# Kernel tuning notes

Measured on AMD Instinct MI355X. Metric: run time of the kernel, lower is better.

## Reference

```python
import jax, jax.numpy as jnp
import numpy as np

B, H, W = 16, 16, 16
L = 32          # in_capsules
O = 32          # out_capsules
P = 16          # p_size
PD = 4          # p_dim = sqrt(p_size)
ETA = 1.0


def setup_inputs() -> dict:
    key = jax.random.key(0)
    k1, k2, k3 = jax.random.split(key, 3)
    # [B, H, W, L*(P+1)]: first L*P channels are poses, last L are activations in [0,1]
    input_tensor = jax.random.uniform(k1, (B, H, W, L * (P + 1)), dtype=jnp.float32)
    # transform weights: [L, O, 4, 4] (kernel_size=1, shared over spatial positions)
    weights = jax.random.normal(k2, (L, O, PD, PD), dtype=jnp.float32) / np.sqrt(PD)
    activation_bias = jax.random.uniform(k3, (O,), dtype=jnp.float32)
    return {"input_tensor": input_tensor, "weights": weights,
            "activation_bias": activation_bias}


def reference(input_tensor, weights, activation_bias):
    Bs, Hh, Ww, _ = input_tensor.shape
    M = Hh * Ww
    # split poses / activations
    poses = input_tensor[..., : L * P].reshape(Bs, M, L, PD, PD)   # [B, M, L, 4, 4]
    acts = input_tensor[..., L * P:].reshape(Bs, M * L)            # [B, N]
    # votes[b, (m,l), o] = pose[b,m,l] @ W[l,o]  (shared transform, repeated over M)
    votes = jnp.einsum('bmlij,lojk->bmloik', poses, weights)
    votes = votes.reshape(Bs, M * L, O, P)                         # [B, N, O, 16]
    # weight votes by input activations and group per output capsule
    Y = (acts[:, :, None, None] * votes).transpose(0, 2, 1, 3)     # [B, O, N, 16]
    # top-1 right singular vector via gram matrix eigendecomposition (detached)
    gram = jnp.einsum('bonp,bonq->bopq', Y, Y)                     # [B, O, 16, 16]
    _, V = jnp.linalg.eigh(jax.lax.stop_gradient(gram))            # ascending eigvals
    pose_out = V[..., -1]                                          # [B, O, 16]
    # agreement: ||Y u||^2 / ||Y||_F^2
    yu = jnp.einsum('bonp,bop->bon', Y, pose_out)                  # [B, O, N]
    ratio = (yu ** 2).sum(-1) / (Y ** 2).sum((-1, -2))             # [B, O]
    act_out = jax.nn.sigmoid(ETA * (ratio - activation_bias))      # [B, O]
    return act_out, pose_out
```

## Files before the change

kernel.cpp:

```cpp
#include <hip/hip_runtime.h>

#define B_ 16
#define L_ 32
#define O_ 32
#define M_ 256
#define CH_ 544


__device__ __forceinline__ float rl(float v, int lane) {
  return __int_as_float(__builtin_amdgcn_readlane(__float_as_int(v), lane));
}

__device__ __forceinline__ float sum16_rl(float v) {
  float s = rl(v, 0);
#pragma unroll
  for (int j = 1; j < 16; j++) s += rl(v, j);
  return s;
}

__device__ __forceinline__ float frcp(float x) { return __builtin_amdgcn_rcpf(x); }
__device__ __forceinline__ float frsq(float x) { return __builtin_amdgcn_rsqf(x); }


__device__ __forceinline__ float slapy2f(float x, float y) {
  float xa = fabsf(x), ya = fabsf(y);
  float w = fmaxf(xa, ya), z = fminf(xa, ya);
  float q = z * frcp(w);
  float res = w * sqrtf(1.f + q * q);
  return (z == 0.f) ? w : res;
}

__device__ __forceinline__ void slartgf(float f, float g, float* c, float* s, float* r) {
  float t = f * f + g * g;
  float inv = frsq(t);
  float d = t * inv;
  float cg = fabsf(f) * inv;
  float rg = copysignf(d, f);
  float sg = g * copysignf(inv, f);
  bool g0 = (g == 0.f), f0 = (f == 0.f);
  *c = g0 ? 1.f : (f0 ? 0.f : cg);
  *s = g0 ? 0.f : (f0 ? copysignf(1.f, g) : sg);
  *r = g0 ? f : (f0 ? fabsf(g) : rg);
}

__device__ __forceinline__ void slaev2f(float a, float b, float c,
                                        float* rt1, float* rt2, float* cs1, float* sn1) {
  float sm = a + c, df = a - c;
  float adf = fabsf(df);
  float tb = b + b;
  float ab = fabsf(tb);
  float acmx, acmn;
  if (fabsf(a) > fabsf(c)) { acmx = a; acmn = c; } else { acmx = c; acmn = a; }
  float rt;
  if (adf > ab) { float q = ab / adf; rt = adf * sqrtf(1.f + q * q); }
  else if (adf < ab) { float q = adf / ab; rt = ab * sqrtf(1.f + q * q); }
  else rt = ab * sqrtf(2.f);
  int sgn1;
  if (sm < 0.f) { *rt1 = 0.5f * (sm - rt); sgn1 = -1; *rt2 = (acmx / *rt1) * acmn - (b / *rt1) * b; }
  else if (sm > 0.f) { *rt1 = 0.5f * (sm + rt); sgn1 = 1; *rt2 = (acmx / *rt1) * acmn - (b / *rt1) * b; }
  else { *rt1 = 0.5f * rt; *rt2 = -0.5f * rt; sgn1 = 1; }
  float cs; int sgn2;
  if (df >= 0.f) { cs = df + rt; sgn2 = 1; } else { cs = df - rt; sgn2 = -1; }
  float acs = fabsf(cs), c1, s1;
  if (acs > ab) { float ct = -tb / cs; s1 = 1.f / sqrtf(1.f + ct * ct); c1 = ct * s1; }
  else if (ab == 0.f) { c1 = 1.f; s1 = 0.f; }
  else { float tn = -cs / tb; c1 = 1.f / sqrtf(1.f + tn * tn); s1 = tn * c1; }
  if (sgn1 == sgn2) { float tn = c1; c1 = -s1; s1 = tn; }
  *cs1 = c1; *sn1 = s1;
}

__global__ __launch_bounds__(256) void moments_kernel(const float* __restrict__ in,
                                                      float* __restrict__ Tmom) {
  int bl = blockIdx.x;
  int b = bl >> 5, l = bl & 31;
  int t = threadIdx.x;
  int w = t >> 6, lane = t & 63;
  __shared__ __align__(16) float ut[4][16][68];
  __shared__ float red[4][16][16];
  const float* base = in + (size_t)b * (M_ * CH_);
  const float* row = base + (size_t)(w * 64 + lane) * CH_ + l * 16;
  float4 p0 = *(const float4*)(row + 0);
  float4 p1 = *(const float4*)(row + 4);
  float4 p2 = *(const float4*)(row + 8);
  float4 p3 = *(const float4*)(row + 12);
  float a = row[512 - l * 16 + l];
  float (*u)[68] = ut[w];
  u[0][lane] = a * p0.x;  u[1][lane] = a * p0.y;  u[2][lane] = a * p0.z;  u[3][lane] = a * p0.w;
  u[4][lane] = a * p1.x;  u[5][lane] = a * p1.y;  u[6][lane] = a * p1.z;  u[7][lane] = a * p1.w;
  u[8][lane] = a * p2.x;  u[9][lane] = a * p2.y;  u[10][lane] = a * p2.z; u[11][lane] = a * p2.w;
  u[12][lane] = a * p3.x; u[13][lane] = a * p3.y; u[14][lane] = a * p3.z; u[15][lane] = a * p3.w;
  asm volatile("" ::: "memory");
  int c = lane & 15, r0 = lane >> 4;
  float acc0 = 0.f, acc1 = 0.f, acc2 = 0.f, acc3 = 0.f;
#pragma unroll
  for (int m4 = 0; m4 < 64; m4 += 4) {
    float4 cv = *(const float4*)&u[c][m4];
    float4 a0 = *(const float4*)&u[r0][m4];
    float4 a1 = *(const float4*)&u[r0 + 4][m4];
    float4 a2 = *(const float4*)&u[r0 + 8][m4];
    float4 a3 = *(const float4*)&u[r0 + 12][m4];
    acc0 += a0.x * cv.x + a0.y * cv.y + a0.z * cv.z + a0.w * cv.w;
    acc1 += a1.x * cv.x + a1.y * cv.y + a1.z * cv.z + a1.w * cv.w;
    acc2 += a2.x * cv.x + a2.y * cv.y + a2.z * cv.z + a2.w * cv.w;
    acc3 += a3.x * cv.x + a3.y * cv.y + a3.z * cv.z + a3.w * cv.w;
  }
  red[w][r0][c] = acc0;
  red[w][r0 + 4][c] = acc1;
  red[w][r0 + 8][c] = acc2;
  red[w][r0 + 12][c] = acc3;
  __syncthreads();
  int rr_ = t >> 4, cc_ = t & 15;
  float s = (red[0][rr_][cc_] + red[1][rr_][cc_]) + (red[2][rr_][cc_] + red[3][rr_][cc_]);
  Tmom[bl * 256 + t] = s;
}

__global__ __launch_bounds__(64) void gram_eig_kernel(const float* __restrict__ Tmom,
                                                      const float* __restrict__ Wt,
                                                      const float* __restrict__ bias,
                                                      float* __restrict__ out) {
  int bo = blockIdx.x;
  int b = bo >> 5, o = bo & 31;
  int lane = threadIdx.x;

  __shared__ __align__(16) float4 Wall4[128];
  __shared__ __align__(16) float4 Tsh4[4 * 18];
  __shared__ float A[16][17];
  __shared__ __align__(16) float Zt[16][16];

  float biasv = bias[o];

  const float4* Wt4 = (const float4*)Wt;
#pragma unroll
  for (int k = 0; k < 2; k++) {
    int idx = lane + 64 * k;
    int l = idx >> 2, part = idx & 3;
    Wall4[idx] = Wt4[(l * 32 + o) * 4 + part];
  }
  asm volatile("" ::: "memory");

  int p = lane >> 2;
  int i_ = p >> 2, k_ = p & 3;
  int i2 = lane & 3;
  float gx = 0.f, gy = 0.f, gz = 0.f, gw = 0.f;
  const float4* T4 = (const float4*)(Tmom + (size_t)(b * 32) * 256);
  const float* WallF = (const float*)Wall4;
  float4 t0 = T4[0 * 64 + lane], t1 = T4[1 * 64 + lane];
  float4 t2 = T4[2 * 64 + lane], t3 = T4[3 * 64 + lane];
  for (int l = 0; l < 32; l++) {
    Tsh4[(lane >> 4) * 18 + (lane & 15)] = t0;
    asm volatile("" ::: "memory");
    t0 = t1; t1 = t2; t2 = t3;
    if (l + 4 < 32) t3 = T4[(l + 4) * 64 + lane];
    float4 wq0 = Wall4[l * 4 + 0], wq1 = Wall4[l * 4 + 1];
    float4 wq2 = Wall4[l * 4 + 2], wq3 = Wall4[l * 4 + 3];
#pragma unroll
    for (int jj = 0; jj < 4; jj++) {
      float4 trow = Tsh4[i_ * 18 + jj * 4 + i2];
      float ux = trow.x * wq0.x + trow.y * wq1.x + trow.z * wq2.x + trow.w * wq3.x;
      float uy = trow.x * wq0.y + trow.y * wq1.y + trow.z * wq2.y + trow.w * wq3.y;
      float uz = trow.x * wq0.z + trow.y * wq1.z + trow.z * wq2.z + trow.w * wq3.z;
      float uw = trow.x * wq0.w + trow.y * wq1.w + trow.z * wq2.w + trow.w * wq3.w;
      float wk = WallF[l * 16 + jj * 4 + k_];
      gx += wk * ux; gy += wk * uy; gz += wk * uz; gw += wk * uw;
    }
    asm volatile("" ::: "memory");
  }
  {
    int q0 = i2 * 4;
    A[p][q0 + 0] = gx; A[p][q0 + 1] = gy; A[p][q0 + 2] = gz; A[p][q0 + 3] = gw;
  }
  asm volatile("" ::: "memory");

  int c16 = lane & 15;
  float a[16];
#pragma unroll
  for (int r = 0; r < 16; r++) a[r] = A[r][c16];

  float trace;
  {
    float diag = 0.f;
#pragma unroll
    for (int r = 0; r < 16; r++) if (c16 == r) diag = a[r];
    trace = sum16_rl((lane < 16) ? diag : 0.f);
  }

  float dreg = 0.f, ereg = 0.f, taureg = 0.f;
  float hv[14];
#pragma unroll
  for (int i = 0; i < 15; i++) {
    float cn = 0.f;
#pragma unroll
    for (int r = i + 2; r < 16; r++) cn += a[r] * a[r];
    float xn2 = rl(cn, i);
    float alpha = rl(a[i + 1], i);
    float taui = 0.f;
    float vc = 0.f;
    if (xn2 == 0.f) {
      if (lane == i) ereg = alpha;
    } else {
      float xnorm = sqrtf(xn2);
      float beta = -copysignf(slapy2f(alpha, xnorm), alpha);
      taui = (beta - alpha) / beta;
      float rs = 1.f / (alpha - beta);
      if (lane == i) ereg = beta;
      vc = (lane == i + 1) ? 1.f : ((lane >= i + 2 && lane < 16) ? a[i] * rs : 0.f);
      float vb[16];
#pragma unroll
      for (int r = i + 1; r < 16; r++) vb[r] = rl(vc, r);
      float acc = 0.f;
#pragma unroll
      for (int r = i + 1; r < 16; r++) acc += a[r] * vb[r];
      float wc = (lane >= i + 1 && lane < 16) ? taui * acc : 0.f;
      float wb[16];
#pragma unroll
      for (int r = i + 1; r < 16; r++) wb[r] = rl(wc, r);
      float dot = 0.f;
#pragma unroll
      for (int r = i + 1; r < 16; r++) dot += vb[r] * wb[r];
      float alph2 = -0.5f * taui * dot;
      wc += alph2 * vc;
#pragma unroll
      for (int r = i + 1; r < 16; r++) wb[r] += alph2 * vb[r];
#pragma unroll
      for (int r = i + 1; r < 16; r++) a[r] -= vb[r] * wc + wb[r] * vc;
    }
    if (i < 14) hv[i] = vc;
    if (lane == i) taureg = taui;
  }
#pragma unroll
  for (int r = 0; r < 16; r++) if (c16 == r) dreg = a[r];
  if (lane >= 16) dreg = 0.f;

  float z[16];
#pragma unroll
  for (int r = 0; r < 16; r++) z[r] = (lane == r) ? 1.f : 0.f;
#pragma unroll
  for (int i = 13; i >= 0; i--) {
    float taui = rl(taureg, i);
    if (taui != 0.f) {
      float vbq[16];
      float s = 0.f;
#pragma unroll
      for (int r = i + 1; r < 16; r++) { vbq[r] = rl(hv[i], r); s += vbq[r] * z[r]; }
      s *= taui;
#pragma unroll
      for (int r = i + 1; r < 16; r++) z[r] -= vbq[r] * s;
    }
  }
  if (lane < 16) {
    float4* zt4 = (float4*)&Zt[lane][0];
    zt4[0] = make_float4(z[0], z[1], z[2], z[3]);
    zt4[1] = make_float4(z[4], z[5], z[6], z[7]);
    zt4[2] = make_float4(z[8], z[9], z[10], z[11]);
    zt4[3] = make_float4(z[12], z[13], z[14], z[15]);
  }
  asm volatile("" ::: "memory");

  float zz[16];
#pragma unroll
  for (int k2 = 0; k2 < 16; k2++) zz[k2] = Zt[k2][c16];

  const float eps = 5.9604645e-08f;
  const float eps2 = eps * eps;
  const float safmin = 1.17549435e-38f;
  int l1 = 0, jtot = 0;
  const int nmaxit = 480;
  float dsh = __shfl(dreg, (lane + 1) & 63, 64);

  while (l1 < 16) {
    if (l1 > 0) { if (lane == l1 - 1) ereg = 0.f; }
    bool co = (lane < 15) &&
              ((ereg == 0.f) ||
               (fabsf(ereg) <= __builtin_amdgcn_sqrtf(fabsf(dreg)) *
                                   __builtin_amdgcn_sqrtf(fabsf(dsh)) * eps));
    unsigned long long bm = __ballot(co) & ~((1ull << l1) - 1ull);
    int m = bm ? (__ffsll(bm) - 1) : 15;
    if (m < 15) { if (lane == m) ereg = 0.f; }
    int l = l1, lend = m;
    l1 = m + 1;
    if (lend == l) continue;
    {
      float dl = rl(dreg, l), dle = rl(dreg, lend);
      if (fabsf(dle) < fabsf(dl)) { int tq = l; l = lend; lend = tq; }
    }

    if (lend > l) {
      for (;;) {
        bool cj = (lane < 15) && ((ereg * ereg) <= eps2 * fabsf(dreg) * fabsf(dsh) + safmin);
        int mq;
        if (l != lend) {
          unsigned long long bb2 = __ballot(cj) & ((1ull << lend) - 1ull) & ~((1ull << l) - 1ull);
          mq = bb2 ? (__ffsll(bb2) - 1) : lend;
        } else mq = lend;
        if (mq < lend) { if (lane == mq) ereg = 0.f; }
        if (mq == l) { l++; if (l <= lend) continue; break; }
        if (mq == l + 1) {
          float d_l = rl(dreg, l), e_l = rl(ereg, l), d_l1 = rl(dreg, l + 1);
          float rt1, rt2, cc, ss;
          slaev2f(d_l, e_l, d_l1, &rt1, &rt2, &cc, &ss);
#pragma unroll
          for (int k = 0; k < 15; k++) if (k == l) {
            float z1 = zz[k + 1], z0v = zz[k];
            zz[k + 1] = cc * z1 - ss * z0v;
            zz[k] = ss * z1 + cc * z0v;
          }
          if (lane == l) { dreg = rt1; ereg = 0.f; dsh = rt2; }
          if (lane == l + 1) dreg = rt2;
          if (lane == l - 1) dsh = rt1;
          l += 2; if (l <= lend) continue; break;
        }
        if (jtot == nmaxit) break;
        jtot++;
        float d0 = dreg, e0 = ereg;
        float pp = rl(d0, l);
        float e_lv = rl(e0, l);
        float gg = (rl(d0, l + 1) - pp) * 0.5f * frcp(e_lv);
        float rr = slapy2f(gg, 1.f);
        gg = rl(d0, mq) - pp + e_lv * frcp(gg + copysignf(rr, gg));
        float ss_ = 1.f, cc_ = 1.f;
        pp = 0.f;
#pragma unroll
        for (int i = 14; i >= 0; i--) {
          if (i <= mq - 1 && i >= l) {
            float e_i = rl(e0, i), d_i = rl(d0, i), d_i1 = rl(d0, i + 1);
            float ff = ss_ * e_i, bb = cc_ * e_i;
            slartgf(gg, ff, &cc_, &ss_, &rr);
            if (i != mq - 1) { if (lane == i + 1) ereg = rr; }
            gg = d_i1 - pp;
            rr = (d_i - gg) * ss_ + 2.f * cc_ * bb;
            pp = ss_ * rr;
            float dnew = gg + pp;
            if (lane == i + 1) dreg = dnew;
            if (lane == i) dsh = dnew;
            gg = cc_ * rr - bb;
            float z1 = zz[i + 1], z0v = zz[i];
            zz[i + 1] = cc_ * z1 + ss_ * z0v;
            zz[i] = -ss_ * z1 + cc_ * z0v;
          }
        }
        float dlv = rl(d0, l) - pp;
        if (lane == l) { dreg = dlv; ereg = gg; }
        if (lane == l - 1) dsh = dlv;
      }
    } else {
      for (;;) {
        bool cj = (lane < 15) && ((ereg * ereg) <= eps2 * fabsf(dreg) * fabsf(dsh) + safmin);
        int mq;
        if (l != lend) {
          unsigned long long bb2 = __ballot(cj) & ((1ull << l) - 1ull) & ~((1ull << lend) - 1ull);
          mq = bb2 ? (63 - __clzll(bb2) + 1) : lend;
        } else mq = lend;
        if (mq > lend) { if (lane == mq - 1) ereg = 0.f; }
        if (mq == l) { l--; if (l >= lend) continue; break; }
        if (mq == l - 1) {
          float d_lm1 = rl(dreg, l - 1), e_lm1 = rl(ereg, l - 1), d_l = rl(dreg, l);
          float rt1, rt2, cc, ss;
          slaev2f(d_lm1, e_lm1, d_l, &rt1, &rt2, &cc, &ss);
#pragma unroll
          for (int k = 0; k < 15; k++) if (k == l - 1) {
            float z1 = zz[k + 1], z0v = zz[k];
            zz[k + 1] = cc * z1 - ss * z0v;
            zz[k] = ss * z1 + cc * z0v;
          }
          if (lane == l - 1) { dreg = rt1; ereg = 0.f; dsh = rt2; }
          if (lane == l) dreg = rt2;
          if (lane == l - 2) dsh = rt1;
          l -= 2; if (l >= lend) continue; break;
        }
        if (jtot == nmaxit) break;
        jtot++;
        float d0 = dreg, e0 = ereg;
        float pp = rl(d0, l);
        float e_lm1 = rl(e0, l - 1);
        float gg = (rl(d0, l - 1) - pp) * 0.5f * frcp(e_lm1);
        float rr = slapy2f(gg, 1.f);
        gg = rl(d0, mq) - pp + e_lm1 * frcp(gg + copysignf(rr, gg));
        float ss_ = 1.f, cc_ = 1.f;
        pp = 0.f;
#pragma unroll
        for (int i = 0; i <= 14; i++) {
          if (i >= mq && i <= l - 1) {
            float e_i = rl(e0, i), d_i = rl(d0, i), d_i1 = rl(d0, i + 1);
            float ff = ss_ * e_i, bb = cc_ * e_i;
            slartgf(gg, ff, &cc_, &ss_, &rr);
            if (i != mq) { if (lane == i - 1) ereg = rr; }
            gg = d_i - pp;
            rr = (d_i1 - gg) * ss_ + 2.f * cc_ * bb;
            pp = ss_ * rr;
            float dnew = gg + pp;
            if (lane == i) dreg = dnew;
            if (lane == i - 1) dsh = dnew;
            gg = cc_ * rr - bb;
            float z1 = zz[i + 1], z0v = zz[i];
            zz[i + 1] = cc_ * z1 - ss_ * z0v;
            zz[i] = ss_ * z1 + cc_ * z0v;
          }
        }
        float dlv = rl(d0, l) - pp;
        if (lane == l) dreg = dlv;
        if (lane == l - 1) { ereg = gg; dsh = dlv; }
      }
    }
  }

  float mx = rl(dreg, 0);
  int k = 0;
#pragma unroll
  for (int j = 1; j < 16; j++) {
    float dj = rl(dreg, j);
    if (dj > mx) { mx = dj; k = j; }
  }
  float ratio = mx / trace;
  float act = 1.f / (1.f + expf(-(ratio - biasv)));
  float zk = zz[0];
#pragma unroll
  for (int j = 1; j < 16; j++) zk = (k == j) ? zz[j] : zk;
  if (lane < 16) out[512 + bo * 16 + lane] = zk;
  if (lane == 0) out[bo] = act;
}

extern "C" void kernel_launch(void* const* d_in, const int* in_sizes, int n_in,
                              void* d_out, int out_size, void* d_ws, size_t ws_size,
                              hipStream_t stream) {
  const float* in = (const float*)d_in[0];
  const float* w = (const float*)d_in[1];
  const float* bias = (const float*)d_in[2];
  float* out = (float*)d_out;
  float* Tmom = (float*)d_ws;

  moments_kernel<<<B_ * L_, 256, 0, stream>>>(in, Tmom);
  gram_eig_kernel<<<B_ * O_, 64, 0, stream>>>(Tmom, w, bias, out);
}
```

Before: 131.7 us.

## Fuse moments and eigen kernels with per-batch atomic counter barrier

Merges the two launches into one persistent-style kernel of 256 blocks. Each block computes two moment tiles, then signals a per-batch atomic counter. Two waves spin until all 16 blocks of that batch have finished, then each solves one gram/eigen problem. This removes the second kernel launch and its gap, at the cost of a hipMemsetAsync, spin-waiting that depends on all blocks being co-resident, and half the threads sitting idle during the eigen phase.

```diff
diff --git a/kernel.cpp b/kernel.cpp
--- a/kernel.cpp
+++ b/kernel.cpp
@@ -5,6 +5,7 @@
 #define O_ 32
 #define M_ 256
 #define CH_ 544
+#define TMOM_BYTES (512 * 256 * 4)
 
 
 __device__ __forceinline__ float rl(float v, int lane) {
@@ -69,203 +70,13 @@
   *cs1 = c1; *sn1 = s1;
 }
 
-__global__ __launch_bounds__(256) void moments_kernel(const float* __restrict__ in,
-                                                      float* __restrict__ Tmom) {
-  int bl = blockIdx.x;
-  int b = bl >> 5, l = bl & 31;
-  int t = threadIdx.x;
-  int w = t >> 6, lane = t & 63;
-  __shared__ __align__(16) float ut[4][16][68];
-  __shared__ float red[4][16][16];
-  const float* base = in + (size_t)b * (M_ * CH_);
-  const float* row = base + (size_t)(w * 64 + lane) * CH_ + l * 16;
-  float4 p0 = *(const float4*)(row + 0);
-  float4 p1 = *(const float4*)(row + 4);
-  float4 p2 = *(const float4*)(row + 8);
-  float4 p3 = *(const float4*)(row + 12);
-  float a = row[512 - l * 16 + l];
-  float (*u)[68] = ut[w];
-  u[0][lane] = a * p0.x;  u[1][lane] = a * p0.y;  u[2][lane] = a * p0.z;  u[3][lane] = a * p0.w;
-  u[4][lane] = a * p1.x;  u[5][lane] = a * p1.y;  u[6][lane] = a * p1.z;  u[7][lane] = a * p1.w;
-  u[8][lane] = a * p2.x;  u[9][lane] = a * p2.y;  u[10][lane] = a * p2.z; u[11][lane] = a * p2.w;
-  u[12][lane] = a * p3.x; u[13][lane] = a * p3.y; u[14][lane] = a * p3.z; u[15][lane] = a * p3.w;
-  asm volatile("" ::: "memory");
-  int c = lane & 15, r0 = lane >> 4;
-  float acc0 = 0.f, acc1 = 0.f, acc2 = 0.f, acc3 = 0.f;
-#pragma unroll
-  for (int m4 = 0; m4 < 64; m4 += 4) {
-    float4 cv = *(const float4*)&u[c][m4];
-    float4 a0 = *(const float4*)&u[r0][m4];
-    float4 a1 = *(const float4*)&u[r0 + 4][m4];
-    float4 a2 = *(const float4*)&u[r0 + 8][m4];
-    float4 a3 = *(const float4*)&u[r0 + 12][m4];
-    acc0 += a0.x * cv.x + a0.y * cv.y + a0.z * cv.z + a0.w * cv.w;
-    acc1 += a1.x * cv.x + a1.y * cv.y + a1.z * cv.z + a1.w * cv.w;
-    acc2 += a2.x * cv.x + a2.y * cv.y + a2.z * cv.z + a2.w * cv.w;
-    acc3 += a3.x * cv.x + a3.y * cv.y + a3.z * cv.z + a3.w * cv.w;
-  }
-  red[w][r0][c] = acc0;
-  red[w][r0 + 4][c] = acc1;
-  red[w][r0 + 8][c] = acc2;
-  red[w][r0 + 12][c] = acc3;
-  __syncthreads();
-  int rr_ = t >> 4, cc_ = t & 15;
-  float s = (red[0][rr_][cc_] + red[1][rr_][cc_]) + (red[2][rr_][cc_] + red[3][rr_][cc_]);
-  Tmom[bl * 256 + t] = s;
-}
-
-__global__ __launch_bounds__(64) void gram_eig_kernel(const float* __restrict__ Tmom,
-                                                      const float* __restrict__ Wt,
-                                                      const float* __restrict__ bias,
-                                                      float* __restrict__ out) {
-  int bo = blockIdx.x;
-  int b = bo >> 5, o = bo & 31;
-  int lane = threadIdx.x;
-
-  __shared__ __align__(16) float4 Wall4[128];
-  __shared__ __align__(16) float4 Tsh4[4 * 18];
-  __shared__ float A[16][17];
-  __shared__ __align__(16) float Zt[16][16];
-
-  float biasv = bias[o];
-
-  const float4* Wt4 = (const float4*)Wt;
-#pragma unroll
-  for (int k = 0; k < 2; k++) {
-    int idx = lane + 64 * k;
-    int l = idx >> 2, part = idx & 3;
-    Wall4[idx] = Wt4[(l * 32 + o) * 4 + part];
-  }
-  asm volatile("" ::: "memory");
-
-  int p = lane >> 2;
-  int i_ = p >> 2, k_ = p & 3;
-  int i2 = lane & 3;
-  float gx = 0.f, gy = 0.f, gz = 0.f, gw = 0.f;
-  const float4* T4 = (const float4*)(Tmom + (size_t)(b * 32) * 256);
-  const float* WallF = (const float*)Wall4;
-  float4 t0 = T4[0 * 64 + lane], t1 = T4[1 * 64 + lane];
-  float4 t2 = T4[2 * 64 + lane], t3 = T4[3 * 64 + lane];
-  for (int l = 0; l < 32; l++) {
-    Tsh4[(lane >> 4) * 18 + (lane & 15)] = t0;
-    asm volatile("" ::: "memory");
-    t0 = t1; t1 = t2; t2 = t3;
-    if (l + 4 < 32) t3 = T4[(l + 4) * 64 + lane];
-    float4 wq0 = Wall4[l * 4 + 0], wq1 = Wall4[l * 4 + 1];
-    float4 wq2 = Wall4[l * 4 + 2], wq3 = Wall4[l * 4 + 3];
-#pragma unroll
-    for (int jj = 0; jj < 4; jj++) {
-      float4 trow = Tsh4[i_ * 18 + jj * 4 + i2];
-      float ux = trow.x * wq0.x + trow.y * wq1.x + trow.z * wq2.x + trow.w * wq3.x;
-      float uy = trow.x * wq0.y + trow.y * wq1.y + trow.z * wq2.y + trow.w * wq3.y;
-      float uz = trow.x * wq0.z + trow.y * wq1.z + trow.z * wq2.z + trow.w * wq3.z;
-      float uw = trow.x * wq0.w + trow.y * wq1.w + trow.z * wq2.w + trow.w * wq3.w;
-      float wk = WallF[l * 16 + jj * 4 + k_];
-      gx += wk * ux; gy += wk * uy; gz += wk * uz; gw += wk * uw;
-    }
-    asm volatile("" ::: "memory");
-  }
-  {
-    int q0 = i2 * 4;
-    A[p][q0 + 0] = gx; A[p][q0 + 1] = gy; A[p][q0 + 2] = gz; A[p][q0 + 3] = gw;
-  }
-  asm volatile("" ::: "memory");
-
-  int c16 = lane & 15;
-  float a[16];
-#pragma unroll
-  for (int r = 0; r < 16; r++) a[r] = A[r][c16];
-
-  float trace;
-  {
-    float diag = 0.f;
-#pragma unroll
-    for (int r = 0; r < 16; r++) if (c16 == r) diag = a[r];
-    trace = sum16_rl((lane < 16) ? diag : 0.f);
-  }
-
-  float dreg = 0.f, ereg = 0.f, taureg = 0.f;
-  float hv[14];
-#pragma unroll
-  for (int i = 0; i < 15; i++) {
-    float cn = 0.f;
-#pragma unroll
-    for (int r = i + 2; r < 16; r++) cn += a[r] * a[r];
-    float xn2 = rl(cn, i);
-    float alpha = rl(a[i + 1], i);
-    float taui = 0.f;
-    float vc = 0.f;
-    if (xn2 == 0.f) {
-      if (lane == i) ereg = alpha;
-    } else {
-      float xnorm = sqrtf(xn2);
-      float beta = -copysignf(slapy2f(alpha, xnorm), alpha);
-      taui = (beta - alpha) / beta;
-      float rs = 1.f / (alpha - beta);
-      if (lane == i) ereg = beta;
-      vc = (lane == i + 1) ? 1.f : ((lane >= i + 2 && lane < 16) ? a[i] * rs : 0.f);
-      float vb[16];
-#pragma unroll
-      for (int r = i + 1; r < 16; r++) vb[r] = rl(vc, r);
-      float acc = 0.f;
-#pragma unroll
-      for (int r = i + 1; r < 16; r++) acc += a[r] * vb[r];
-      float wc = (lane >= i + 1 && lane < 16) ? taui * acc : 0.f;
-      float wb[16];
-#pragma unroll
-      for (int r = i + 1; r < 16; r++) wb[r] = rl(wc, r);
-      float dot = 0.f;
-#pragma unroll
-      for (int r = i + 1; r < 16; r++) dot += vb[r] * wb[r];
-      float alph2 = -0.5f * taui * dot;
-      wc += alph2 * vc;
-#pragma unroll
-      for (int r = i + 1; r < 16; r++) wb[r] += alph2 * vb[r];
-#pragma unroll
-      for (int r = i + 1; r < 16; r++) a[r] -= vb[r] * wc + wb[r] * vc;
-    }
-    if (i < 14) hv[i] = vc;
-    if (lane == i) taureg = taui;
-  }
-#pragma unroll
-  for (int r = 0; r < 16; r++) if (c16 == r) dreg = a[r];
-  if (lane >= 16) dreg = 0.f;
-
-  float z[16];
-#pragma unroll
-  for (int r = 0; r < 16; r++) z[r] = (lane == r) ? 1.f : 0.f;
-#pragma unroll
-  for (int i = 13; i >= 0; i--) {
-    float taui = rl(taureg, i);
-    if (taui != 0.f) {
-      float vbq[16];
-      float s = 0.f;
-#pragma unroll
-      for (int r = i + 1; r < 16; r++) { vbq[r] = rl(hv[i], r); s += vbq[r] * z[r]; }
-      s *= taui;
-#pragma unroll
-      for (int r = i + 1; r < 16; r++) z[r] -= vbq[r] * s;
-    }
-  }
-  if (lane < 16) {
-    float4* zt4 = (float4*)&Zt[lane][0];
-    zt4[0] = make_float4(z[0], z[1], z[2], z[3]);
-    zt4[1] = make_float4(z[4], z[5], z[6], z[7]);
-    zt4[2] = make_float4(z[8], z[9], z[10], z[11]);
-    zt4[3] = make_float4(z[12], z[13], z[14], z[15]);
-  }
-  asm volatile("" ::: "memory");
-
-  float zz[16];
-#pragma unroll
-  for (int k2 = 0; k2 < 16; k2++) zz[k2] = Zt[k2][c16];
-
+__device__ __forceinline__ void steqr16(int lane, float& dreg, float& ereg,
+                                        float& dsh, float (&zz)[16]) {
   const float eps = 5.9604645e-08f;
   const float eps2 = eps * eps;
   const float safmin = 1.17549435e-38f;
   int l1 = 0, jtot = 0;
   const int nmaxit = 480;
-  float dsh = __shfl(dreg, (lane + 1) & 63, 64);
 
   while (l1 < 16) {
     if (l1 > 0) { if (lane == l1 - 1) ereg = 0.f; }
@@ -402,6 +213,197 @@
       }
     }
   }
+}
+
+__device__ __forceinline__ void moments_tile(const float* __restrict__ in,
+                                             float* __restrict__ Tmom,
+                                             int bl, int t,
+                                             float (*ut)[16][68],
+                                             float (*red)[16][16]) {
+  int b = bl >> 5, l = bl & 31;
+  int w = t >> 6, lane = t & 63;
+  const float* base = in + (size_t)b * (M_ * CH_);
+  const float* row = base + (size_t)(w * 64 + lane) * CH_ + l * 16;
+  float4 p0 = *(const float4*)(row + 0);
+  float4 p1 = *(const float4*)(row + 4);
+  float4 p2 = *(const float4*)(row + 8);
+  float4 p3 = *(const float4*)(row + 12);
+  float a = row[512 - l * 16 + l];
+  float (*u)[68] = ut[w];
+  u[0][lane] = a * p0.x;  u[1][lane] = a * p0.y;  u[2][lane] = a * p0.z;  u[3][lane] = a * p0.w;
+  u[4][lane] = a * p1.x;  u[5][lane] = a * p1.y;  u[6][lane] = a * p1.z;  u[7][lane] = a * p1.w;
+  u[8][lane] = a * p2.x;  u[9][lane] = a * p2.y;  u[10][lane] = a * p2.z; u[11][lane] = a * p2.w;
+  u[12][lane] = a * p3.x; u[13][lane] = a * p3.y; u[14][lane] = a * p3.z; u[15][lane] = a * p3.w;
+  asm volatile("" ::: "memory");
+  int c = lane & 15, r0 = lane >> 4;
+  float acc0 = 0.f, acc1 = 0.f, acc2 = 0.f, acc3 = 0.f;
+#pragma unroll
+  for (int m4 = 0; m4 < 64; m4 += 4) {
+    float4 cv = *(const float4*)&u[c][m4];
+    float4 a0 = *(const float4*)&u[r0][m4];
+    float4 a1 = *(const float4*)&u[r0 + 4][m4];
+    float4 a2 = *(const float4*)&u[r0 + 8][m4];
+    float4 a3 = *(const float4*)&u[r0 + 12][m4];
+    acc0 += a0.x * cv.x + a0.y * cv.y + a0.z * cv.z + a0.w * cv.w;
+    acc1 += a1.x * cv.x + a1.y * cv.y + a1.z * cv.z + a1.w * cv.w;
+    acc2 += a2.x * cv.x + a2.y * cv.y + a2.z * cv.z + a2.w * cv.w;
+    acc3 += a3.x * cv.x + a3.y * cv.y + a3.z * cv.z + a3.w * cv.w;
+  }
+  red[w][r0][c] = acc0;
+  red[w][r0 + 4][c] = acc1;
+  red[w][r0 + 8][c] = acc2;
+  red[w][r0 + 12][c] = acc3;
+  __syncthreads();
+  int rr_ = t >> 4, cc_ = t & 15;
+  float s = (red[0][rr_][cc_] + red[1][rr_][cc_]) + (red[2][rr_][cc_] + red[3][rr_][cc_]);
+  Tmom[bl * 256 + t] = s;
+}
+
+__device__ __forceinline__ void gram_eig_one(const float* __restrict__ Tmom,
+                                             const float* __restrict__ Wt,
+                                             const float* __restrict__ bias,
+                                             float* __restrict__ out,
+                                             int bo, int lane,
+                                             float4* Wall4, float4* Tsh4,
+                                             float (*A)[17], float (*Zt)[16]) {
+  int b = bo >> 5, o = bo & 31;
+
+  float biasv = bias[o];
+
+  const float4* Wt4 = (const float4*)Wt;
+#pragma unroll
+  for (int k = 0; k < 2; k++) {
+    int idx = lane + 64 * k;
+    int l = idx >> 2, part = idx & 3;
+    Wall4[idx] = Wt4[(l * 32 + o) * 4 + part];
+  }
+  asm volatile("" ::: "memory");
+
+  int p = lane >> 2;
+  int i_ = p >> 2, k_ = p & 3;
+  int i2 = lane & 3;
+  float gx = 0.f, gy = 0.f, gz = 0.f, gw = 0.f;
+  const float4* T4 = (const float4*)(Tmom + (size_t)(b * 32) * 256);
+  const float* WallF = (const float*)Wall4;
+  float4 t0 = T4[0 * 64 + lane], t1 = T4[1 * 64 + lane];
+  float4 t2 = T4[2 * 64 + lane], t3 = T4[3 * 64 + lane];
+  for (int l = 0; l < 32; l++) {
+    Tsh4[(lane >> 4) * 18 + (lane & 15)] = t0;
+    asm volatile("" ::: "memory");
+    t0 = t1; t1 = t2; t2 = t3;
+    if (l + 4 < 32) t3 = T4[(l + 4) * 64 + lane];
+    float4 wq0 = Wall4[l * 4 + 0], wq1 = Wall4[l * 4 + 1];
+    float4 wq2 = Wall4[l * 4 + 2], wq3 = Wall4[l * 4 + 3];
+#pragma unroll
+    for (int jj = 0; jj < 4; jj++) {
+      float4 trow = Tsh4[i_ * 18 + jj * 4 + i2];
+      float ux = trow.x * wq0.x + trow.y * wq1.x + trow.z * wq2.x + trow.w * wq3.x;
+      float uy = trow.x * wq0.y + trow.y * wq1.y + trow.z * wq2.y + trow.w * wq3.y;
+      float uz = trow.x * wq0.z + trow.y * wq1.z + trow.z * wq2.z + trow.w * wq3.z;
+      float uw = trow.x * wq0.w + trow.y * wq1.w + trow.z * wq2.w + trow.w * wq3.w;
+      float wk = WallF[l * 16 + jj * 4 + k_];
+      gx += wk * ux; gy += wk * uy; gz += wk * uz; gw += wk * uw;
+    }
+    asm volatile("" ::: "memory");
+  }
+  {
+    int q0 = i2 * 4;
+    A[p][q0 + 0] = gx; A[p][q0 + 1] = gy; A[p][q0 + 2] = gz; A[p][q0 + 3] = gw;
+  }
+  asm volatile("" ::: "memory");
+
+  int c16 = lane & 15;
+  float a[16];
+#pragma unroll
+  for (int r = 0; r < 16; r++) a[r] = A[r][c16];
+
+  float trace;
+  {
+    float diag = 0.f;
+#pragma unroll
+    for (int r = 0; r < 16; r++) if (c16 == r) diag = a[r];
+    trace = sum16_rl((lane < 16) ? diag : 0.f);
+  }
+
+  float dreg = 0.f, ereg = 0.f, taureg = 0.f;
+  float hv[14];
+#pragma unroll
+  for (int i = 0; i < 15; i++) {
+    float cn = 0.f;
+#pragma unroll
+    for (int r = i + 2; r < 16; r++) cn += a[r] * a[r];
+    float xn2 = rl(cn, i);
+    float alpha = rl(a[i + 1], i);
+    float taui = 0.f;
+    float vc = 0.f;
+    if (xn2 == 0.f) {
+      if (lane == i) ereg = alpha;
+    } else {
+      float xnorm = sqrtf(xn2);
+      float beta = -copysignf(slapy2f(alpha, xnorm), alpha);
+      taui = (beta - alpha) / beta;
+      float rs = 1.f / (alpha - beta);
+      if (lane == i) ereg = beta;
+      vc = (lane == i + 1) ? 1.f : ((lane >= i + 2 && lane < 16) ? a[i] * rs : 0.f);
+      float vb[16];
+#pragma unroll
+      for (int r = i + 1; r < 16; r++) vb[r] = rl(vc, r);
+      float acc = 0.f;
+#pragma unroll
+      for (int r = i + 1; r < 16; r++) acc += a[r] * vb[r];
+      float wc = (lane >= i + 1 && lane < 16) ? taui * acc : 0.f;
+      float wb[16];
+#pragma unroll
+      for (int r = i + 1; r < 16; r++) wb[r] = rl(wc, r);
+      float dot = 0.f;
+#pragma unroll
+      for (int r = i + 1; r < 16; r++) dot += vb[r] * wb[r];
+      float alph2 = -0.5f * taui * dot;
+      wc += alph2 * vc;
+#pragma unroll
+      for (int r = i + 1; r < 16; r++) wb[r] += alph2 * vb[r];
+#pragma unroll
+      for (int r = i + 1; r < 16; r++) a[r] -= vb[r] * wc + wb[r] * vc;
+    }
+    if (i < 14) hv[i] = vc;
+    if (lane == i) taureg = taui;
+  }
+#pragma unroll
+  for (int r = 0; r < 16; r++) if (c16 == r) dreg = a[r];
+  if (lane >= 16) dreg = 0.f;
+
+  float z[16];
+#pragma unroll
+  for (int r = 0; r < 16; r++) z[r] = (lane == r) ? 1.f : 0.f;
+#pragma unroll
+  for (int i = 13; i >= 0; i--) {
+    float taui = rl(taureg, i);
+    if (taui != 0.f) {
+      float vbq[16];
+      float s = 0.f;
+#pragma unroll
+      for (int r = i + 1; r < 16; r++) { vbq[r] = rl(hv[i], r); s += vbq[r] * z[r]; }
+      s *= taui;
+#pragma unroll
+      for (int r = i + 1; r < 16; r++) z[r] -= vbq[r] * s;
+    }
+  }
+  if (lane < 16) {
+    float4* zt4 = (float4*)&Zt[lane][0];
+    zt4[0] = make_float4(z[0], z[1], z[2], z[3]);
+    zt4[1] = make_float4(z[4], z[5], z[6], z[7]);
+    zt4[2] = make_float4(z[8], z[9], z[10], z[11]);
+    zt4[3] = make_float4(z[12], z[13], z[14], z[15]);
+  }
+  asm volatile("" ::: "memory");
+
+  float zz[16];
+#pragma unroll
+  for (int k2 = 0; k2 < 16; k2++) zz[k2] = Zt[k2][c16];
+
+  float dsh = __shfl(dreg, (lane + 1) & 63, 64);
+
+  steqr16(lane, dreg, ereg, dsh, zz);
 
   float mx = rl(dreg, 0);
   int k = 0;
@@ -417,6 +419,64 @@
   for (int j = 1; j < 16; j++) zk = (k == j) ? zz[j] : zk;
   if (lane < 16) out[512 + bo * 16 + lane] = zk;
   if (lane == 0) out[bo] = act;
+}
+
+__global__ __launch_bounds__(256) void moments_kernel(const float* __restrict__ in,
+                                                      float* __restrict__ Tmom) {
+  __shared__ __align__(16) float ut[4][16][68];
+  __shared__ float red[4][16][16];
+  moments_tile(in, Tmom, blockIdx.x, threadIdx.x, ut, red);
+}
+
+__global__ __launch_bounds__(64) void gram_eig_kernel(const float* __restrict__ Tmom,
+                                                      const float* __restrict__ Wt,
+                                                      const float* __restrict__ bias,
+                                                      float* __restrict__ out) {
+  __shared__ __align__(16) float4 Wall4[128];
+  __shared__ __align__(16) float4 Tsh4[4 * 18];
+  __shared__ float A[16][17];
+  __shared__ __align__(16) float Zt[16][16];
+  gram_eig_one(Tmom, Wt, bias, out, blockIdx.x, threadIdx.x, Wall4, Tsh4, A, Zt);
+}
+
+__global__ __launch_bounds__(256) void fused_kernel(const float* __restrict__ in,
+                                                    const float* __restrict__ Wt,
+                                                    const float* __restrict__ bias,
+                                                    float* __restrict__ out,
+                                                    float* __restrict__ Tmom,
+                                                    int* __restrict__ cnt) {
+  __shared__ __align__(16) float ut[4][16][68];
+  __shared__ float red[4][16][16];
+  __shared__ __align__(16) float4 Wall4[2][128];
+  __shared__ __align__(16) float4 Tsh4[2][4 * 18];
+  __shared__ float A[2][16][17];
+  __shared__ __align__(16) float Zt[2][16][16];
+
+  int k = blockIdx.x;
+  int b = k >> 4;
+  int t = threadIdx.x;
+
+  for (int tile = 0; tile < 2; ++tile) {
+    moments_tile(in, Tmom, 2 * k + tile, t, ut, red);
+    __syncthreads();
+  }
+
+  if (t == 0) {
+    __threadfence();
+    __hip_atomic_fetch_add(&cnt[b], 1, __ATOMIC_RELEASE, __HIP_MEMORY_SCOPE_AGENT);
+  }
+
+  if (t >= 128) return;
+  int wv = t >> 6, lane = t & 63;
+
+  if (lane == 0) {
+    while (__hip_atomic_load(&cnt[b], __ATOMIC_ACQUIRE, __HIP_MEMORY_SCOPE_AGENT) < 16)
+      __builtin_amdgcn_s_sleep(2);
+  }
+  __threadfence();
+
+  gram_eig_one(Tmom, Wt, bias, out, 2 * k + wv, lane,
+               Wall4[wv], Tsh4[wv], A[wv], Zt[wv]);
 }
 
 extern "C" void kernel_launch(void* const* d_in, const int* in_sizes, int n_in,
@@ -428,6 +488,12 @@
   float* out = (float*)d_out;
   float* Tmom = (float*)d_ws;
 
-  moments_kernel<<<B_ * L_, 256, 0, stream>>>(in, Tmom);
-  gram_eig_kernel<<<B_ * O_, 64, 0, stream>>>(Tmom, w, bias, out);
-}
+  if (ws_size >= (size_t)TMOM_BYTES + 64) {
+    int* cnt = (int*)((char*)d_ws + TMOM_BYTES);
+    hipMemsetAsync(cnt, 0, 64, stream);
+    fused_kernel<<<256, 256, 0, stream>>>(in, w, bias, out, Tmom, cnt);
+  } else {
+    moments_kernel<<<B_ * L_, 256, 0, stream>>>(in, Tmom);
+    gram_eig_kernel<<<B_ * O_, 64, 0, stream>>>(Tmom, w, bias, out);
+  }
+}
```

Measured after the change: 162.0 us. 23.0% more time.
